# Kernel optimization log

Hardware: AMD Instinct MI355X
Metric: run time of the kernel (lower is better)

The kernel has to match this reference:

```python
import jax, jax.numpy as jnp
import numpy as np
import math

L_SEQ = 1048576  # 2**20 time steps
N_LAT = 64       # latent_dim


def setup_inputs() -> dict:
    key = jax.random.key(0)
    ks = jax.random.split(key, 5)
    u = jax.random.normal(ks[0], (L_SEQ,), dtype=jnp.float32)
    # Stable Hurwitz A so the discretized transition Abar has spectral radius < 1
    # (torch's rand(N,N) init overflows for large L; math of the layer is unchanged).
    A = (0.05 * jax.random.normal(ks[1], (N_LAT, N_LAT), dtype=jnp.float32)
         - 2.0 * jnp.eye(N_LAT, dtype=jnp.float32))
    B = jax.random.uniform(ks[2], (N_LAT, 1), dtype=jnp.float32)
    C = jax.random.uniform(ks[3], (1, N_LAT), dtype=jnp.float32)
    D = jax.random.uniform(ks[4], (1, 1), dtype=jnp.float32)
    dt = jnp.float32(0.05)  # learned log-step, here a fixed sampled value
    return {"u": u, "A": A, "B": B, "C": C, "D": D, "dt": dt}


def reference(u, A, B, C, D, dt):
    n = A.shape[0]
    I = jnp.eye(n, dtype=A.dtype)
    # Bilinear discretization: Abar = (I - dt/2 A)^-1 (I + dt/2 A), Bbar = (I - dt/2 A)^-1 (dt B)
    Bl = jnp.linalg.inv(I - (dt / 2) * A)
    Abar = Bl @ (I + (dt / 2) * A)          # (N, N)
    Bbar = Bl @ (dt * B)                     # (N, 1)
    L = u.shape[0]

    # K_l = C @ Abar^l @ Bbar, computed with a single linear scan (same math as
    # the per-step matrix_power loop, evaluated iteratively).
    def step(x, _):
        k = (C @ x)[0, 0]
        return Abar @ x, k
    _, K = jax.lax.scan(step, Bbar, None, length=L)  # K: (L,)

    # FFT causal convolution (mode=False path)
    nfft = 2 ** int(math.ceil(math.log2(2 * L)))
    y = jnp.fft.irfft(jnp.fft.rfft(K, n=nfft) * jnp.fft.rfft(u, n=nfft), n=nfft)[:L]
    # torch broadcasting: (L,) + (1,1)*(L,) -> (1, L)
    return y + D * u
```

## Files before the change

kernel.cpp:

```cpp
#include <hip/hip_runtime.h>


#define NN    64
#define STR   72
#define TKC   80
#define NA    20

#define BT    512
#define RR    8
#define OUTB  (BT * RR)
#define UTILE (TKC + OUTB + 8)
#define U4    (UTILE / 4)
#define ULDS  4352

typedef _Float16 half8 __attribute__((ext_vector_type(8)));
typedef _Float16 half4 __attribute__((ext_vector_type(4)));
typedef __attribute__((ext_vector_type(4))) float f32x4;

__device__ __forceinline__ float rdlane(float v, int m) {
  return __int_as_float(__builtin_amdgcn_readlane(__float_as_int(v), m));
}
__device__ __forceinline__ f32x4 MFMA(half8 a, half8 b, f32x4 c) {
  return __builtin_amdgcn_mfma_f32_16x16x32_f16(a, b, c, 0, 0, 0);
}
__device__ __forceinline__ int swz(int m) {
  return m ^ (((m >> 5) & 7) << 2);
}

template<int MODE>
__device__ __forceinline__ void mmf8(
    const _Float16 (*Ah)[STR], const _Float16 (*Bh)[STR],
    _Float16 (*Oh)[STR], _Float16 (*Th)[STR], float (*Gf)[68], int t) {
  const int lane = t & 63;
  const int rs = (t >> 6) & 3;
  const int ch = t >> 8;
  const int rA = (rs << 4) + (lane & 15);
  const int kb = (lane >> 4) << 3;
  half8 ah[2], bh[2][2];
#pragma unroll
  for (int kc = 0; kc < 2; ++kc)
    ah[kc] = *(const half8*)&Ah[rA][kc * 32 + kb];
#pragma unroll
  for (int ci = 0; ci < 2; ++ci) {
    const int rB = ((2 * ch + ci) << 4) + (lane & 15);
#pragma unroll
    for (int kc = 0; kc < 2; ++kc)
      bh[ci][kc] = *(const half8*)&Bh[rB][kc * 32 + kb];
  }
  __syncthreads();
  {
    const f32x4 zz = {0.f, 0.f, 0.f, 0.f};
    f32x4 acc[2] = {zz, zz};
#pragma unroll
    for (int ci = 0; ci < 2; ++ci)
#pragma unroll
      for (int kc = 0; kc < 2; ++kc)
        acc[ci] = MFMA(ah[kc], bh[ci][kc], acc[ci]);
    const int rbase = (rs << 4) + ((lane >> 4) << 2);
#pragma unroll
    for (int ci = 0; ci < 2; ++ci) {
      const int col = ((2 * ch + ci) << 4) + (lane & 15);
      if (MODE == 3) {
        float4 o;
        o.x = acc[ci][0]; o.y = acc[ci][1];
        o.z = acc[ci][2]; o.w = acc[ci][3];
        *(float4*)&Gf[col][rbase] = o;
      } else {
        half4 tv;
#pragma unroll
        for (int ri = 0; ri < 4; ++ri) {
          const int r = rbase + ri;
          const float f = acc[ci][ri];
          if (MODE == 0) {
            const float x = (float)Ah[r][col];
            const float z = ((r == col) ? 1.f : 0.f) + 2.f * x + f;
            Oh[r][col] = (_Float16)z;
            const float q = f + ((r == col) ? 1.f : 0.f);
            tv[ri] = (_Float16)q;
          } else {
            tv[ri] = (_Float16)f;
            Oh[r][col] = tv[ri];
          }
        }
        *(half4*)&Th[col][rbase] = tv;
      }
    }
  }
  __syncthreads();
}

__device__ __forceinline__ float scanstep_f32(float wv, const float (*Gf)[68],
                                              int c) {
  float s0 = 0.f, s1 = 0.f, s2 = 0.f, s3 = 0.f;
#pragma unroll
  for (int m4 = 0; m4 < NN; m4 += 4) {
    const float4 g = *(const float4*)&Gf[c][m4];
    s0 = fmaf(rdlane(wv, m4 + 0), g.x, s0);
    s1 = fmaf(rdlane(wv, m4 + 1), g.y, s1);
    s2 = fmaf(rdlane(wv, m4 + 2), g.z, s2);
    s3 = fmaf(rdlane(wv, m4 + 3), g.w, s3);
  }
  return (s0 + s1) + (s2 + s3);
}

__device__ __forceinline__ float scanstep_f16(float wv,
    const _Float16 (*GT)[STR], int c) {
  float s0 = 0.f, s1 = 0.f, s2 = 0.f, s3 = 0.f;
#pragma unroll
  for (int m8 = 0; m8 < NN; m8 += 8) {
    const half8 hv = *(const half8*)&GT[c][m8];
#pragma unroll
    for (int j = 0; j < 8; ++j) {
      const float g = (float)hv[j];
      if ((j & 3) == 0) s0 = fmaf(rdlane(wv, m8 + j), g, s0);
      else if ((j & 3) == 1) s1 = fmaf(rdlane(wv, m8 + j), g, s1);
      else if ((j & 3) == 2) s2 = fmaf(rdlane(wv, m8 + j), g, s2);
      else s3 = fmaf(rdlane(wv, m8 + j), g, s3);
    }
  }
  return (s0 + s1) + (s2 + s3);
}

__device__ __forceinline__ float rowdot(const _Float16 (*M)[STR],
                                        const float* v, int i) {
  float s = 0.f;
#pragma unroll
  for (int k8 = 0; k8 < NN; k8 += 8) {
    const half8 hv = *(const half8*)&M[i][k8];
#pragma unroll
    for (int j = 0; j < 8; ++j)
      s = fmaf((float)hv[j], v[k8 + j], s);
  }
  return s;
}

__global__ __launch_bounds__(512, 1) void fused_kernel(
    const float* __restrict__ u, const float* __restrict__ A,
    const float* __restrict__ Bv, const float* __restrict__ Cv,
    const float* __restrict__ Dp, const float* __restrict__ dtp,
    float* __restrict__ y, int L) {
  __shared__ __align__(16) _Float16 P1[NN][STR];
  __shared__ __align__(16) _Float16 P2[NN][STR];
  __shared__ __align__(16) float ulds[ULDS];
  __shared__ __align__(16) float Wl[NA][68];
  __shared__ __align__(16) float VTr[4][NN];
  __shared__ __align__(16) float Kl[TKC];
  __shared__ float Bls[NN], Cls[NN];

  float (*Gf)[68] = (float(*)[68])&ulds[0];

  const int t = threadIdx.x;
  const int l0 = (int)blockIdx.x * OUTB;
  const int ubase = l0 - TKC - 8;
  const float dtv = dtp[0];

  float4 av0, av1, av2, av3;
  if (t < 256) {
    const float* Ap = A + t * 16;
    av0 = *(const float4*)(Ap + 0);
    av1 = *(const float4*)(Ap + 4);
    av2 = *(const float4*)(Ap + 8);
    av3 = *(const float4*)(Ap + 12);
  }
  if (t < NN) { Bls[t] = Bv[t]; Cls[t] = Cv[t]; }

  float4 uv0, uv1, uv2;
  {
    auto ldu = [&](int i) {
      const int g = ubase + 4 * i;
      float4 v;
      if (g >= 0) {
        v = *(const float4*)(u + g);
      } else {
        v.x = (g + 0 >= 0) ? u[g + 0] : 0.f;
        v.y = (g + 1 >= 0) ? u[g + 1] : 0.f;
        v.z = (g + 2 >= 0) ? u[g + 2] : 0.f;
        v.w = (g + 3 >= 0) ? u[g + 3] : 0.f;
      }
      return v;
    };
    uv0 = ldu(t);
    uv1 = ldu(t + 512);
    if (t < U4 - 1024) uv2 = ldu(t + 1024);
  }

  if (t < 256) {
    const float h2 = 0.5f * dtv;
    const int row = t >> 2, col0 = (t & 3) << 4;
    float xx[16];
    *(float4*)&xx[0] = av0; *(float4*)&xx[4] = av1;
    *(float4*)&xx[8] = av2; *(float4*)&xx[12] = av3;
    half8 h0, h1;
#pragma unroll
    for (int j = 0; j < 8; ++j) h0[j] = (_Float16)(h2 * xx[j]);
#pragma unroll
    for (int j = 0; j < 8; ++j) h1[j] = (_Float16)(h2 * xx[8 + j]);
    *(half8*)&P1[row][col0] = h0;
    *(half8*)&P1[row][col0 + 8] = h1;
#pragma unroll
    for (int j = 0; j < 8; ++j) P2[col0 + j][row] = h0[j];
#pragma unroll
    for (int j = 0; j < 8; ++j) P2[col0 + 8 + j][row] = h1[j];
  }
  __syncthreads();

  mmf8<0>(P1, P2, P1, P2, nullptr, t);
  mmf8<1>(P1, P2, P1, P2, nullptr, t);

  if (t < NN) {
    const float s = Bls[t] + rowdot(P1, Bls, t);
    VTr[0][t] = 0.5f * dtv * s;
  }
  __syncthreads();
  if (t < NN) VTr[1][t] = rowdot(P1, &VTr[0][0], t);
  __syncthreads();

  mmf8<1>(P1, P2, P1, P2, nullptr, t);

  {
    float r2 = 0.f;
    if (t < 128) r2 = rowdot(P1, &VTr[t >> 6][0], t & 63);
    __syncthreads();
    if (t < 128) VTr[2 + (t >> 6)][t & 63] = r2;
    __syncthreads();
  }

  mmf8<1>(P1, P2, P1, P2, nullptr, t);
  mmf8<3>(P1, P2, nullptr, nullptr, Gf, t);

  if (t < 128) {
    const int c = t & 63;
    const int odd = t >> 6;
    float wv = Cls[c];
    if (odd == 0) {
      Wl[0][c] = wv;
#pragma unroll 1
      for (int s = 0; s < 9; ++s) {
        wv = scanstep_f32(wv, Gf, c);
        Wl[2 * (s + 1)][c] = wv;
      }
    } else {
      wv = scanstep_f16(wv, P2, c);
      Wl[1][c] = wv;
#pragma unroll 1
      for (int s = 0; s < 9; ++s) {
        wv = scanstep_f32(wv, Gf, c);
        Wl[3 + 2 * s][c] = wv;
      }
    }
  }
  __syncthreads();

  if (t < TKC) {
    const int a = t >> 2, b = t & 3;
    float s = 0.f;
#pragma unroll
    for (int i = 0; i < NN; i += 4) {
      const float4 w4 = *(const float4*)&Wl[a][i];
      const float4 v4 = *(const float4*)&VTr[b][i];
      s += w4.x * v4.x + w4.y * v4.y + w4.z * v4.z + w4.w * v4.w;
    }
    Kl[t] = s;
  }

  *(float4*)&ulds[swz(4 * t)] = uv0;
  *(float4*)&ulds[swz(4 * (t + 512))] = uv1;
  if (t < U4 - 1024) *(float4*)&ulds[swz(4 * (t + 1024))] = uv2;
  __syncthreads();

  {
    float acc[RR];
#pragma unroll
    for (int i = 0; i < RR; ++i) acc[i] = 0.f;

    const int mtop = TKC + 8 + t * RR;
    float hA[8], hB[8];
    *(float4*)&hB[0] = *(const float4*)&ulds[swz(mtop)];
    *(float4*)&hB[4] = *(const float4*)&ulds[swz(mtop + 4)];
    *(float4*)&hA[0] = *(const float4*)&ulds[swz(mtop - 8)];
    *(float4*)&hA[4] = *(const float4*)&ulds[swz(mtop - 4)];

#pragma unroll 1
    for (int j = 0; j < TKC; j += 16) {
      {
        const float4 k0 = *(const float4*)&Kl[j];
        const float4 k1 = *(const float4*)&Kl[j + 4];
        const float kk[8] = {k0.x, k0.y, k0.z, k0.w, k1.x, k1.y, k1.z, k1.w};
#pragma unroll
        for (int jj = 0; jj < 8; ++jj)
#pragma unroll
          for (int i = 0; i < RR; ++i) {
            const int d = i - jj;
            acc[i] += kk[jj] * (d >= 0 ? hB[d] : hA[8 + d]);
          }
      }
      {
        const int mb = mtop - j - 16;
        *(float4*)&hB[0] = *(const float4*)&ulds[swz(mb)];
        *(float4*)&hB[4] = *(const float4*)&ulds[swz(mb + 4)];
      }
      {
        const float4 k0 = *(const float4*)&Kl[j + 8];
        const float4 k1 = *(const float4*)&Kl[j + 12];
        const float kk[8] = {k0.x, k0.y, k0.z, k0.w, k1.x, k1.y, k1.z, k1.w};
#pragma unroll
        for (int jj = 0; jj < 8; ++jj)
#pragma unroll
          for (int i = 0; i < RR; ++i) {
            const int d = i - jj;
            acc[i] += kk[jj] * (d >= 0 ? hA[d] : hB[8 + d]);
          }
      }
      {
        const int mb = mtop - j - 24;
        *(float4*)&hA[0] = *(const float4*)&ulds[swz(mb)];
        *(float4*)&hA[4] = *(const float4*)&ulds[swz(mb + 4)];
      }
    }

    const float Dv = Dp[0];
    {
      const float4 q0 = *(const float4*)&ulds[swz(mtop)];
      const float4 q1 = *(const float4*)&ulds[swz(mtop + 4)];
      const float uq[8] = {q0.x, q0.y, q0.z, q0.w, q1.x, q1.y, q1.z, q1.w};
#pragma unroll
      for (int i = 0; i < RR; ++i) acc[i] += Dv * uq[i];
    }
    float4 o0, o1;
    o0.x = acc[0]; o0.y = acc[1]; o0.z = acc[2]; o0.w = acc[3];
    o1.x = acc[4]; o1.y = acc[5]; o1.z = acc[6]; o1.w = acc[7];
    *(float4*)&y[l0 + t * RR] = o0;
    *(float4*)&y[l0 + t * RR + 4] = o1;
  }
}

extern "C" void kernel_launch(void* const* d_in, const int* in_sizes, int n_in,
                              void* d_out, int out_size, void* d_ws, size_t ws_size,
                              hipStream_t stream) {
  const float* u   = (const float*)d_in[0];
  const float* A   = (const float*)d_in[1];
  const float* Bv  = (const float*)d_in[2];
  const float* Cv  = (const float*)d_in[3];
  const float* Dp  = (const float*)d_in[4];
  const float* dtp = (const float*)d_in[5];
  float* y = (float*)d_out;
  const int L = in_sizes[0];

  fused_kernel<<<L / OUTB, BT, 0, stream>>>(u, A, Bv, Cv, Dp, dtp, y, L);
}
```

Baseline: 16.85 us.

## Ping-pong matrix buffers to drop barriers and overlap u tile staging

Replaces in-place squaring of the P1/P2 matrices with four LDS buffers used in ping-pong fashion. This removes the mid-mmf8 __syncthreads and several barriers around the rowdot steps. The Gf scratch moves from the u tile region into the matrix buffers, so the u tile can be written to LDS during the serial Krylov scan instead of afterwards. The cost is more LDS for matrices, and the correctness of the removed barriers now rests on the buffer alternation.

```diff
diff --git a/kernel.cpp b/kernel.cpp
--- a/kernel.cpp
+++ b/kernel.cpp
@@ -11,7 +11,7 @@
 #define OUTB  (BT * RR)
 #define UTILE (TKC + OUTB + 8)
 #define U4    (UTILE / 4)
-#define ULDS  4352
+#define ULDS  4224
 
 typedef _Float16 half8 __attribute__((ext_vector_type(8)));
 typedef _Float16 half4 __attribute__((ext_vector_type(4)));
@@ -29,8 +29,8 @@
 
 template<int MODE>
 __device__ __forceinline__ void mmf8(
-    const _Float16 (*Ah)[STR], const _Float16 (*Bh)[STR],
-    _Float16 (*Oh)[STR], _Float16 (*Th)[STR], float (*Gf)[68], int t) {
+    const _Float16 (*Arm)[STR], const _Float16 (*Bt)[STR],
+    _Float16 (*Orm)[STR], _Float16 (*Ot)[STR], float (*Gf)[68], int t) {
   const int lane = t & 63;
   const int rs = (t >> 6) & 3;
   const int ch = t >> 8;
@@ -39,51 +39,47 @@
   half8 ah[2], bh[2][2];
 #pragma unroll
   for (int kc = 0; kc < 2; ++kc)
-    ah[kc] = *(const half8*)&Ah[rA][kc * 32 + kb];
+    ah[kc] = *(const half8*)&Arm[rA][kc * 32 + kb];
 #pragma unroll
   for (int ci = 0; ci < 2; ++ci) {
     const int rB = ((2 * ch + ci) << 4) + (lane & 15);
 #pragma unroll
     for (int kc = 0; kc < 2; ++kc)
-      bh[ci][kc] = *(const half8*)&Bh[rB][kc * 32 + kb];
-  }
-  __syncthreads();
-  {
-    const f32x4 zz = {0.f, 0.f, 0.f, 0.f};
-    f32x4 acc[2] = {zz, zz};
-#pragma unroll
-    for (int ci = 0; ci < 2; ++ci)
-#pragma unroll
-      for (int kc = 0; kc < 2; ++kc)
-        acc[ci] = MFMA(ah[kc], bh[ci][kc], acc[ci]);
-    const int rbase = (rs << 4) + ((lane >> 4) << 2);
-#pragma unroll
-    for (int ci = 0; ci < 2; ++ci) {
-      const int col = ((2 * ch + ci) << 4) + (lane & 15);
-      if (MODE == 3) {
-        float4 o;
-        o.x = acc[ci][0]; o.y = acc[ci][1];
-        o.z = acc[ci][2]; o.w = acc[ci][3];
-        *(float4*)&Gf[col][rbase] = o;
-      } else {
-        half4 tv;
-#pragma unroll
-        for (int ri = 0; ri < 4; ++ri) {
-          const int r = rbase + ri;
-          const float f = acc[ci][ri];
-          if (MODE == 0) {
-            const float x = (float)Ah[r][col];
-            const float z = ((r == col) ? 1.f : 0.f) + 2.f * x + f;
-            Oh[r][col] = (_Float16)z;
-            const float q = f + ((r == col) ? 1.f : 0.f);
-            tv[ri] = (_Float16)q;
-          } else {
-            tv[ri] = (_Float16)f;
-            Oh[r][col] = tv[ri];
-          }
+      bh[ci][kc] = *(const half8*)&Bt[rB][kc * 32 + kb];
+  }
+  const f32x4 zz = {0.f, 0.f, 0.f, 0.f};
+  f32x4 acc[2] = {zz, zz};
+#pragma unroll
+  for (int ci = 0; ci < 2; ++ci)
+#pragma unroll
+    for (int kc = 0; kc < 2; ++kc)
+      acc[ci] = MFMA(ah[kc], bh[ci][kc], acc[ci]);
+  const int rbase = (rs << 4) + ((lane >> 4) << 2);
+#pragma unroll
+  for (int ci = 0; ci < 2; ++ci) {
+    const int col = ((2 * ch + ci) << 4) + (lane & 15);
+    if (MODE == 3) {
+      float4 o;
+      o.x = acc[ci][0]; o.y = acc[ci][1];
+      o.z = acc[ci][2]; o.w = acc[ci][3];
+      *(float4*)&Gf[col][rbase] = o;
+    } else {
+      half4 tv;
+#pragma unroll
+      for (int ri = 0; ri < 4; ++ri) {
+        const int r = rbase + ri;
+        const float f = acc[ci][ri];
+        if (MODE == 0) {
+          const float x = (float)Arm[r][col];
+          const float z = ((r == col) ? 1.f : 0.f) + 2.f * x + f;
+          Orm[r][col] = (_Float16)z;
+          tv[ri] = (_Float16)(f + ((r == col) ? 1.f : 0.f));
+        } else {
+          tv[ri] = (_Float16)f;
+          Orm[r][col] = tv[ri];
         }
-        *(half4*)&Th[col][rbase] = tv;
-      }
+      }
+      *(half4*)&Ot[col][rbase] = tv;
     }
   }
   __syncthreads();
@@ -139,15 +135,14 @@
     const float* __restrict__ Bv, const float* __restrict__ Cv,
     const float* __restrict__ Dp, const float* __restrict__ dtp,
     float* __restrict__ y, int L) {
-  __shared__ __align__(16) _Float16 P1[NN][STR];
-  __shared__ __align__(16) _Float16 P2[NN][STR];
+  __shared__ __align__(16) _Float16 MP[4][NN][STR];
   __shared__ __align__(16) float ulds[ULDS];
   __shared__ __align__(16) float Wl[NA][68];
   __shared__ __align__(16) float VTr[4][NN];
   __shared__ __align__(16) float Kl[TKC];
   __shared__ float Bls[NN], Cls[NN];
 
-  float (*Gf)[68] = (float(*)[68])&ulds[0];
+  float (*Gf)[68] = (float(*)[68])&MP[2][0][0];
 
   const int t = threadIdx.x;
   const int l0 = (int)blockIdx.x * OUTB;
@@ -195,38 +190,34 @@
     for (int j = 0; j < 8; ++j) h0[j] = (_Float16)(h2 * xx[j]);
 #pragma unroll
     for (int j = 0; j < 8; ++j) h1[j] = (_Float16)(h2 * xx[8 + j]);
-    *(half8*)&P1[row][col0] = h0;
-    *(half8*)&P1[row][col0 + 8] = h1;
-#pragma unroll
-    for (int j = 0; j < 8; ++j) P2[col0 + j][row] = h0[j];
-#pragma unroll
-    for (int j = 0; j < 8; ++j) P2[col0 + 8 + j][row] = h1[j];
-  }
-  __syncthreads();
-
-  mmf8<0>(P1, P2, P1, P2, nullptr, t);
-  mmf8<1>(P1, P2, P1, P2, nullptr, t);
+    *(half8*)&MP[0][row][col0] = h0;
+    *(half8*)&MP[0][row][col0 + 8] = h1;
+#pragma unroll
+    for (int j = 0; j < 8; ++j) MP[1][col0 + j][row] = h0[j];
+#pragma unroll
+    for (int j = 0; j < 8; ++j) MP[1][col0 + 8 + j][row] = h1[j];
+  }
+  __syncthreads();
+
+  mmf8<0>(MP[0], MP[1], MP[2], MP[3], nullptr, t);
+  mmf8<1>(MP[2], MP[3], MP[0], MP[1], nullptr, t);
 
   if (t < NN) {
-    const float s = Bls[t] + rowdot(P1, Bls, t);
+    const float s = Bls[t] + rowdot(MP[0], Bls, t);
     VTr[0][t] = 0.5f * dtv * s;
   }
   __syncthreads();
-  if (t < NN) VTr[1][t] = rowdot(P1, &VTr[0][0], t);
-  __syncthreads();
-
-  mmf8<1>(P1, P2, P1, P2, nullptr, t);
-
-  {
-    float r2 = 0.f;
-    if (t < 128) r2 = rowdot(P1, &VTr[t >> 6][0], t & 63);
-    __syncthreads();
-    if (t < 128) VTr[2 + (t >> 6)][t & 63] = r2;
-    __syncthreads();
-  }
-
-  mmf8<1>(P1, P2, P1, P2, nullptr, t);
-  mmf8<3>(P1, P2, nullptr, nullptr, Gf, t);
+  if (t < NN) VTr[1][t] = rowdot(MP[0], &VTr[0][0], t);
+
+  mmf8<1>(MP[0], MP[1], MP[2], MP[3], nullptr, t);
+
+  if (t < 128) {
+    const int i = t & 63, q = t >> 6;
+    VTr[2 + q][i] = rowdot(MP[2], &VTr[q][0], i);
+  }
+
+  mmf8<1>(MP[2], MP[3], MP[0], MP[1], nullptr, t);
+  mmf8<3>(MP[0], MP[1], nullptr, nullptr, Gf, t);
 
   if (t < 128) {
     const int c = t & 63;
@@ -240,7 +231,7 @@
         Wl[2 * (s + 1)][c] = wv;
       }
     } else {
-      wv = scanstep_f16(wv, P2, c);
+      wv = scanstep_f16(wv, MP[1], c);
       Wl[1][c] = wv;
 #pragma unroll 1
       for (int s = 0; s < 9; ++s) {
@@ -248,6 +239,12 @@
         Wl[3 + 2 * s][c] = wv;
       }
     }
+    *(float4*)&ulds[swz(4 * t)] = uv0;
+    *(float4*)&ulds[swz(4 * (t + 512))] = uv1;
+    if (t < U4 - 1024) *(float4*)&ulds[swz(4 * (t + 1024))] = uv2;
+  } else {
+    *(float4*)&ulds[swz(4 * t)] = uv0;
+    *(float4*)&ulds[swz(4 * (t + 512))] = uv1;
   }
   __syncthreads();
 
@@ -262,10 +259,6 @@
     }
     Kl[t] = s;
   }
-
-  *(float4*)&ulds[swz(4 * t)] = uv0;
-  *(float4*)&ulds[swz(4 * (t + 512))] = uv1;
-  if (t < U4 - 1024) *(float4*)&ulds[swz(4 * (t + 1024))] = uv2;
   __syncthreads();
 
   {
```

Measured after the change: 16.13 us. 1.04x faster.
